# Kernel tuning notes

Measured on AMD Instinct MI355X. Metric: run time of the kernel, lower is better.

The kernel has to match this reference:

```python
import jax, jax.numpy as jnp
import numpy as np

B, L, D, T, NL = 64, 512, 512, 5000, 2


def setup_inputs() -> dict:
    key = jax.random.key(0)
    k1, k2, k3, k4 = jax.random.split(key, 4)
    enc_output = jax.random.normal(k1, (B, L, D), dtype=jnp.float32)
    # stands in for the row/col-normalized tag co-occurrence matrix (values in [0, 0.01])
    ui_adj = jax.random.uniform(k2, (T, T), dtype=jnp.float32) * 0.01
    # one GCN weight matrix per layer in the layer_stack
    Ws = jax.random.normal(k3, (NL, D, D), dtype=jnp.float32) / np.sqrt(D).astype(np.float32)
    # event ids are 1-indexed in the original (it indexes with e - 1)
    event_type = jax.random.randint(k4, (B, L), 1, T + 1, dtype=jnp.int64)
    slf_attn_mask = jnp.zeros((B, L, L), dtype=bool)
    non_pad_mask = jnp.ones((B, L), dtype=bool)
    return {"enc_output": enc_output, "ui_adj": ui_adj, "Ws": Ws,
            "event_type": event_type, "slf_attn_mask": slf_attn_mask,
            "non_pad_mask": non_pad_mask}


def reference(enc_output, ui_adj, Ws, event_type, slf_attn_mask, non_pad_mask):
    # --- batched per-sample adjacency gather (replaces the Python loop) ---
    idx = event_type - 1                                   # [B, L] 0-indexed
    sub = ui_adj[idx[:, :, None], idx[:, None, :]]         # [B, L, L] = ui_adj[e-1,:][:, e-1]
    diag = ui_adj[idx, idx]                                # [B, L]   = ui_adj[e-1, e-1]
    adj = sub + diag[:, None, :]                           # vector broadcasts across rows, as in torch
    # --- GNN layer stack (hGCN layer ~ relu(A @ X @ W)) ---
    x = enc_output
    for l in range(Ws.shape[0]):                           # small fixed n_layers loop
        x = jax.nn.relu(jnp.einsum('bij,bjd->bid', adj, x) @ Ws[l])
    # --- mean pool over sequence ---
    return x.mean(axis=1)                                  # [B, D]
```

## Files before the change

kernel.cpp:

```cpp
#include <hip/hip_runtime.h>

typedef unsigned short u16;
typedef unsigned int u32;
typedef __bf16 bf16x8 __attribute__((ext_vector_type(8)));
typedef float f32x4 __attribute__((ext_vector_type(4)));
typedef int i32x4 __attribute__((ext_vector_type(4)));
typedef u32 u32x2 __attribute__((ext_vector_type(2)));
typedef u32 u32x4 __attribute__((ext_vector_type(4)));

#define T_ 5000
#define CAP 96

__device__ __forceinline__ u16 f2bf(float f) {
  u32 u = __float_as_uint(f);
  u += 0x7fffu + ((u >> 16) & 1u);
  return (u16)(u >> 16);
}
__device__ __forceinline__ float bf2f(u32 bits16) {
  return __uint_as_float(bits16 << 16);
}

__device__ __forceinline__ void gload_lds16(const u16* g, u16* l) {
  __builtin_amdgcn_global_load_lds(
      (__attribute__((address_space(1))) void*)(u16*)g,
      (__attribute__((address_space(3))) void*)l, 16, 0, 0);
}

__device__ __forceinline__ u32 lds_off(const void* p) {
  return (u32)(uintptr_t)(__attribute__((address_space(3))) const void*)p;
}

__global__ void transpose_cast(const float* __restrict__ src, u16* __restrict__ dst) {
  __shared__ float tile[32][33];
  const int tx = threadIdx.x, ty = threadIdx.y;
  const int a0 = blockIdx.x * 32;
  const int b0 = blockIdx.y * 32;
  const size_t zoff = (size_t)blockIdx.z * (512 * 512);
  const float* s = src + zoff;
  u16* d = dst + zoff;
#pragma unroll
  for (int r = 0; r < 4; ++r)
    tile[ty + r * 8][tx] = s[(size_t)(a0 + ty + r * 8) * 512 + b0 + tx];
  __syncthreads();
#pragma unroll
  for (int r = 0; r < 4; ++r)
    d[(size_t)(b0 + ty + r * 8) * 512 + a0 + tx] = f2bf(tile[tx][ty + r * 8]);
}

__global__ void zero_k(int* __restrict__ cnt) {
  const int t = blockIdx.x * 256 + threadIdx.x;
  if (t < 5001) cnt[t] = 0;
}

__global__ void fill_k(const int* __restrict__ ev, const float* __restrict__ ui,
                       int2* __restrict__ cd, int* __restrict__ cnt,
                       int* __restrict__ list, int* __restrict__ ovf) {
  const int t = blockIdx.x * 256 + threadIdx.x;
  const int r = ev[t] - 1;
  int2 v;
  v.x = r;
  v.y = __float_as_int(ui[(size_t)r * (T_ + 1)]);
  cd[t] = v;
  const int pos = atomicAdd(&cnt[r], 1);
  if (pos < CAP) list[r * CAP + pos] = t;
  else { const int o = atomicAdd(&cnt[5000], 1); ovf[o] = t; }
}

__global__ __launch_bounds__(256)
void grow_gather(const float* __restrict__ ui, const int2* __restrict__ cd,
                 const int* __restrict__ cnt, const int* __restrict__ list,
                 u16* __restrict__ adj) {
  const int r = blockIdx.x;
  int c = cnt[r];
  if (c <= 0) return;
  if (c > CAP) c = CAP;
  __shared__ float row[5000];
  const float* __restrict__ src = ui + (size_t)r * T_;
  for (int t = threadIdx.x; t < 1250; t += 256)
    *(float4*)&row[t * 4] = *(const float4*)&src[t * 4];
  __syncthreads();
  const int j = threadIdx.x * 2;
  const int lb = r * CAP;
  int q = 0;
  for (; q + 2 <= c; q += 2) {
    const int t0 = list[lb + q], t1 = list[lb + q + 1];
    const int b0 = (t0 >> 9) << 9, b1 = (t1 >> 9) << 9;
    const int4 p0 = *(const int4*)&cd[b0 + j];
    const int4 p1 = *(const int4*)&cd[b1 + j];
    const u32 pk0 = (u32)f2bf(row[p0.x] + __int_as_float(p0.y)) |
                    ((u32)f2bf(row[p0.z] + __int_as_float(p0.w)) << 16);
    const u32 pk1 = (u32)f2bf(row[p1.x] + __int_as_float(p1.y)) |
                    ((u32)f2bf(row[p1.z] + __int_as_float(p1.w)) << 16);
    *(u32*)&adj[(size_t)t0 * 512 + j] = pk0;
    *(u32*)&adj[(size_t)t1 * 512 + j] = pk1;
  }
  if (q < c) {
    const int t0 = list[lb + q];
    const int b0 = (t0 >> 9) << 9;
    const int4 p0 = *(const int4*)&cd[b0 + j];
    const u32 pk0 = (u32)f2bf(row[p0.x] + __int_as_float(p0.y)) |
                    ((u32)f2bf(row[p0.z] + __int_as_float(p0.w)) << 16);
    *(u32*)&adj[(size_t)t0 * 512 + j] = pk0;
  }
}

__global__ void ovf_gather(const float* __restrict__ ui, const int2* __restrict__ cd,
                           const int* __restrict__ cnt, const int* __restrict__ ovf,
                           u16* __restrict__ adj) {
  const int n = cnt[5000];
  for (int q = blockIdx.x; q < n; q += gridDim.x) {
    const int t = ovf[q];
    const int base = (t >> 9) << 9;
    const long r = (long)cd[t].x;
    const float* __restrict__ row = ui + r * (long)T_;
    const int j = threadIdx.x * 2;
    const int4 p = *(const int4*)&cd[base + j];
    const u32 pk = (u32)f2bf(row[p.x] + __int_as_float(p.y)) |
                   ((u32)f2bf(row[p.z] + __int_as_float(p.w)) << 16);
    *(u32*)&adj[(size_t)t * 512 + j] = pk;
  }
}

template <int MODE, int BSRC>
__global__ __launch_bounds__(512, 2)
void gemm256(const u16* __restrict__ A, const void* __restrict__ Bv,
             u16* __restrict__ C, size_t strideA, size_t strideB, size_t strideC,
             float* __restrict__ P) {
  extern __shared__ u16 smem[];
  const int tid = threadIdx.x;
  const int lane = tid & 63;
  const int w = tid >> 6;
  const int wm = w >> 2, wn = w & 3;
  const int chunk = gridDim.x >> 3;
  const int wg = blockIdx.x;
  const int mapped = (wg & 7) * chunk + (wg >> 3);
  const int batch = mapped >> 2;
  const int tm = (mapped >> 1) & 1, tn = mapped & 1;
  const int m0 = tm << 8, n0 = tn << 8;
  const u16* __restrict__ Ab = A + (size_t)batch * strideA;

  const u16* gA[2];
  u32 ldA[2];
#pragma unroll
  for (int r = 0; r < 2; ++r) {
    const int c = r * 512 + tid;
    const int L = c * 16;
    const int pp = L >> 7;
    const int off = (L & 127) ^ ((pp & 7) << 4);
    const int m = pp * 2 + (off >> 6);
    const int kb = off & 63;
    gA[r] = Ab + (size_t)(m0 + m) * 512 + (kb >> 1);
    ldA[r] = (u32)((r * 512 + w * 64) * 8);
  }

  const u16* gB[2] = {nullptr, nullptr};
  u32 ldB[2] = {0, 0};
  if (BSRC == 0) {
    const u16* __restrict__ Bb = (const u16*)Bv + (size_t)batch * strideB;
#pragma unroll
    for (int r = 0; r < 2; ++r) {
      const int c = r * 512 + tid;
      const int L = c * 16;
      const int pp = L >> 7;
      const int off = (L & 127) ^ ((pp & 7) << 4);
      const int m = pp * 2 + (off >> 6);
      const int kb = off & 63;
      gB[r] = Bb + (size_t)(n0 + m) * 512 + (kb >> 1);
      ldB[r] = (u32)(32768 + (r * 512 + w * 64) * 8);
    }
  }

  const int dp = tid & 127;
  const int lq = tid >> 7;
  unsigned long long encB = 0;
  u32 boff0 = 0;
  u32x2 bs0[8], bs1[8];
  if (BSRC == 1) {
    encB = (unsigned long long)(uintptr_t)((const float*)Bv + (size_t)batch * strideB);
    boff0 = (u32)(((lq * 8) * 512 + n0 + dp * 2) * 4);
  }

#define BLOAD(t, S)                                                          \
  {                                                                          \
    const u32 ob = boff0 + (u32)(t) * 65536u;                                \
    _Pragma("unroll") for (int i = 0; i < 8; ++i)                            \
        asm volatile("global_load_dwordx2 %0, %1, %2"                        \
                     : "=v"(S[i])                                            \
                     : "v"(ob + (u32)i * 2048u), "s"(encB));                 \
  }

#define CONVERT_B(S)                                                         \
  {                                                                          \
    u32 wrd0[4], wrd1[4];                                                    \
    _Pragma("unroll") for (int jj = 0; jj < 4; ++jj) {                       \
      asm("v_cvt_pk_bf16_f32 %0, %1, %2"                                     \
          : "=v"(wrd0[jj]) : "v"(S[2 * jj].x), "v"(S[2 * jj + 1].x));        \
      asm("v_cvt_pk_bf16_f32 %0, %1, %2"                                     \
          : "=v"(wrd1[jj]) : "v"(S[2 * jj].y), "v"(S[2 * jj + 1].y));        \
    }                                                                        \
    const u32 by0 = (u32)dp * 128u + ((((u32)lq * 16u)) ^ (((u32)dp & 7u) << 4)); \
    const u32 by1 = (u32)dp * 128u + ((64u | ((u32)lq * 16u)) ^ (((u32)dp & 7u) << 4)); \
    u32x4 v0, v1;                                                            \
    v0.x = wrd0[0]; v0.y = wrd0[1]; v0.z = wrd0[2]; v0.w = wrd0[3];          \
    v1.x = wrd1[0]; v1.y = wrd1[1]; v1.z = wrd1[2]; v1.w = wrd1[3];          \
    *(u32x4*)((char*)smem + 65536 + by0) = v0;                               \
    *(u32x4*)((char*)smem + 65536 + by1) = v1;                               \
  }

  const int lr = lane & 15;
  const int kb = (lane >> 4) << 4;
  u32 aOff[8], bOff[4];
#pragma unroll
  for (int m = 0; m < 8; ++m) {
    const int row = wm * 128 + m * 16 + lr;
    aOff[m] = (u32)((row >> 1) * 128 + ((((row & 1) << 6) | kb) ^ (((row >> 1) & 7) << 4)));
  }
#pragma unroll
  for (int n = 0; n < 4; ++n) {
    const int row = wn * 64 + n * 16 + lr;
    bOff[n] = (u32)(65536 + (row >> 1) * 128 + ((((row & 1) << 6) | kb) ^ (((row >> 1) & 7) << 4)));
  }
  const u32 ldsBase = lds_off(smem);

  f32x4 acc[8][4] = {};

  auto stageA = [&](int t) {
    const u32 bo = (u32)(t & 3) * 8192;
#pragma unroll
    for (int r = 0; r < 2; ++r) gload_lds16(gA[r] + t * 32, smem + bo + ldA[r]);
  };
  auto stageB0 = [&](int t) {
    const u32 bo = (u32)(t & 3) * 8192;
#pragma unroll
    for (int r = 0; r < 2; ++r) gload_lds16(gB[r] + t * 32, smem + bo + ldB[r]);
  };

  if (BSRC == 0) {
    stageA(0); stageB0(0); stageA(1); stageB0(1); stageA(2); stageB0(2);
  } else {
    stageA(0); stageA(1); stageA(2);
    BLOAD(0, bs0); BLOAD(1, bs1);
  }

#pragma unroll
  for (int t = 0; t < 16; ++t) {
    if (BSRC == 0) {
      if (t <= 13)      asm volatile("s_waitcnt vmcnt(8)" ::: "memory");
      else if (t == 14) asm volatile("s_waitcnt vmcnt(4)" ::: "memory");
      else              asm volatile("s_waitcnt vmcnt(0)" ::: "memory");
      __builtin_amdgcn_sched_barrier(0);
      if (t + 3 < 16) { stageA(t + 3); stageB0(t + 3); }
      asm volatile("" ::: "memory");
      __builtin_amdgcn_s_barrier();
      asm volatile("" ::: "memory");
    } else {
      if (t == 0)              asm volatile("s_waitcnt vmcnt(8)" ::: "memory");
      else if (t <= 13)        asm volatile("s_waitcnt vmcnt(10)" ::: "memory");
      else if (t == 14)        asm volatile("s_waitcnt vmcnt(8)" ::: "memory");
      else                     asm volatile("s_waitcnt vmcnt(0)" ::: "memory");
      __builtin_amdgcn_sched_barrier(0);
      if (t & 1) { CONVERT_B(bs1); } else { CONVERT_B(bs0); }
      if (t + 3 < 16) stageA(t + 3);
      if (t + 2 < 16) { if (t & 1) { BLOAD(t + 2, bs1); } else { BLOAD(t + 2, bs0); } }
      asm volatile("s_waitcnt lgkmcnt(0)" ::: "memory");
      __builtin_amdgcn_s_barrier();
      asm volatile("" ::: "memory");
    }

    const u32 abase = ldsBase + (u32)(t & 3) * 16384;
    const u32 bbase = (BSRC == 0) ? (ldsBase + (u32)(t & 3) * 16384) : ldsBase;
    i32x4 araw[8], braw[4];
#pragma unroll
    for (int m = 0; m < 8; ++m)
      asm volatile("ds_read_b128 %0, %1" : "=v"(araw[m]) : "v"(abase + aOff[m]));
#pragma unroll
    for (int n = 0; n < 4; ++n)
      asm volatile("ds_read_b128 %0, %1" : "=v"(braw[n]) : "v"(bbase + bOff[n]));
    asm volatile("s_waitcnt lgkmcnt(0)" ::: "memory");
    __builtin_amdgcn_sched_barrier(0);

    __builtin_amdgcn_s_setprio(1);
#pragma unroll
    for (int m = 0; m < 8; ++m)
#pragma unroll
      for (int n = 0; n < 4; ++n)
        acc[m][n] = __builtin_amdgcn_mfma_f32_16x16x32_bf16(
            __builtin_bit_cast(bf16x8, araw[m]),
            __builtin_bit_cast(bf16x8, braw[n]), acc[m][n], 0, 0, 0);
    __builtin_amdgcn_s_setprio(0);
    asm volatile("" ::: "memory");
    __builtin_amdgcn_s_barrier();
    __builtin_amdgcn_sched_barrier(0);
  }
#undef BLOAD
#undef CONVERT_B

  u16* Cb = C + (size_t)batch * strideC;
  if (MODE == 0) {
#pragma unroll
    for (int m = 0; m < 8; ++m) {
      const int row = m0 + wm * 128 + m * 16 + (lane >> 4) * 4;
#pragma unroll
      for (int n = 0; n < 4; ++n) {
        const int col = n0 + wn * 64 + n * 16 + (lane & 15);
        const f32x4 v = acc[m][n];
#pragma unroll
        for (int j = 0; j < 4; ++j)
          Cb[(size_t)(row + j) * 512 + col] = f2bf(v[j]);
      }
    }
  } else if (MODE == 1) {
#pragma unroll
    for (int m = 0; m < 8; ++m) {
      const int i = m0 + wm * 128 + m * 16 + (lane >> 4) * 4;
#pragma unroll
      for (int n = 0; n < 4; ++n) {
        const int d = n0 + wn * 64 + n * 16 + (lane & 15);
        const f32x4 v = acc[m][n];
        uint2 p;
        p.x = (u32)f2bf(fmaxf(v[0], 0.f)) | ((u32)f2bf(fmaxf(v[1], 0.f)) << 16);
        p.y = (u32)f2bf(fmaxf(v[2], 0.f)) | ((u32)f2bf(fmaxf(v[3], 0.f)) << 16);
        *(uint2*)&Cb[(size_t)d * 512 + i] = p;
      }
    }
  } else {
    const int slot = tm * 2 + wm;
#pragma unroll
    for (int n = 0; n < 4; ++n) {
      float s = 0.f;
#pragma unroll
      for (int m = 0; m < 8; ++m) {
        const f32x4 v = acc[m][n];
#pragma unroll
        for (int j = 0; j < 4; ++j) s += fmaxf(v[j], 0.f);
      }
      s += __shfl_xor(s, 16);
      s += __shfl_xor(s, 32);
      if ((lane >> 4) == 0) {
        const int d = n0 + wn * 64 + n * 16 + lane;
        P[((size_t)batch * 4 + slot) * 512 + d] = s;
      }
    }
  }
}

__global__ void reduce_mean(const float* __restrict__ P, float* __restrict__ out) {
  const int t = blockIdx.x * 256 + threadIdx.x;
  const int b = t >> 9, d = t & 511;
  float s = 0.f;
#pragma unroll
  for (int q = 0; q < 4; ++q) s += P[((size_t)b * 4 + q) * 512 + d];
  out[t] = s * (1.0f / 512.0f);
}

extern "C" void kernel_launch(void* const* d_in, const int* in_sizes, int n_in,
                              void* d_out, int out_size, void* d_ws, size_t ws_size,
                              hipStream_t stream) {
  const float* enc = (const float*)d_in[0];
  const float* ui  = (const float*)d_in[1];
  const float* Ws  = (const float*)d_in[2];
  const int*   ev  = (const int*)d_in[3];
  float* out = (float*)d_out;

  char* ws = (char*)d_ws;
  const size_t SLAB = (size_t)64 * 512 * 512 * 2;
  u16* adj  = (u16*)(ws);
  u16* tbuf = (u16*)(ws + SLAB);
  u16* xb   = (u16*)(ws + 2 * SLAB);
  char* p = ws + 3 * SLAB;
  u16* wst  = (u16*)p;  p += (size_t)2 * 512 * 512 * 2;
  int2* cd  = (int2*)p; p += (size_t)32768 * 8;
  int* cnt  = (int*)p;  p += 5008 * 4;
  int* list = (int*)p;  p += (size_t)5000 * CAP * 4;
  int* ovf  = (int*)p;  p += (size_t)32768 * 4;
  float* P  = (float*)p;

  const size_t PS = (size_t)512 * 512;
  const size_t SMEM0 = 131072;
  const size_t SMEM1 = 81920;
  (void)hipFuncSetAttribute(reinterpret_cast<const void*>(gemm256<0, 1>),
                            hipFuncAttributeMaxDynamicSharedMemorySize, (int)SMEM1);
  (void)hipFuncSetAttribute(reinterpret_cast<const void*>(gemm256<1, 0>),
                            hipFuncAttributeMaxDynamicSharedMemorySize, (int)SMEM0);
  (void)hipFuncSetAttribute(reinterpret_cast<const void*>(gemm256<0, 0>),
                            hipFuncAttributeMaxDynamicSharedMemorySize, (int)SMEM0);
  (void)hipFuncSetAttribute(reinterpret_cast<const void*>(gemm256<2, 0>),
                            hipFuncAttributeMaxDynamicSharedMemorySize, (int)SMEM0);

  zero_k<<<20, 256, 0, stream>>>(cnt);
  fill_k<<<128, 256, 0, stream>>>(ev, ui, cd, cnt, list, ovf);
  transpose_cast<<<dim3(16, 16, 2), dim3(32, 8), 0, stream>>>(Ws, wst);
  grow_gather<<<5000, 256, 0, stream>>>(ui, cd, cnt, list, adj);
  ovf_gather<<<8, 256, 0, stream>>>(ui, cd, cnt, ovf, adj);
  gemm256<0, 1><<<256, 512, SMEM1, stream>>>(adj, enc, tbuf, PS, PS, PS, nullptr);
  gemm256<1, 0><<<256, 512, SMEM0, stream>>>(tbuf, wst, xb, PS, 0, PS, nullptr);
  gemm256<0, 0><<<256, 512, SMEM0, stream>>>(adj, xb, tbuf, PS, PS, PS, nullptr);
  gemm256<2, 0><<<256, 512, SMEM0, stream>>>(tbuf, wst + PS, nullptr, PS, 0, 0, P);
  reduce_mean<<<128, 256, 0, stream>>>(P, out);
}
```

Baseline: 141.1 us.

## Switch GEMMs to 32x32x16 MFMA, split LDS waits, and merge small launches

The GEMM inner loop moves from 16x16x32 to 32x32x16 bf16 MFMA tiles, so fewer LDS fragment reads feed the same work. The LDS wait is split so the first half of the MFMAs can start after a partial lgkmcnt wait. The three epilogues are remapped to the 32x32 accumulator layout. Separately, counter zeroing is folded into the weight transpose kernel, and the overflow gather is folded into grow_gather, which also stages its list in LDS and unrolls by four. This removes two kernel launches but makes blocks 0-7 do the overflow work serially.

```diff
diff --git a/kernel.cpp b/kernel.cpp
--- a/kernel.cpp
+++ b/kernel.cpp
@@ -3,7 +3,7 @@
 typedef unsigned short u16;
 typedef unsigned int u32;
 typedef __bf16 bf16x8 __attribute__((ext_vector_type(8)));
-typedef float f32x4 __attribute__((ext_vector_type(4)));
+typedef float f32x16 __attribute__((ext_vector_type(16)));
 typedef int i32x4 __attribute__((ext_vector_type(4)));
 typedef u32 u32x2 __attribute__((ext_vector_type(2)));
 typedef u32 u32x4 __attribute__((ext_vector_type(4)));
@@ -30,7 +30,13 @@
   return (u32)(uintptr_t)(__attribute__((address_space(3))) const void*)p;
 }
 
-__global__ void transpose_cast(const float* __restrict__ src, u16* __restrict__ dst) {
+__device__ __forceinline__ u32 swz(int row, int kb) {
+  return (u32)((row >> 1) * 128 +
+               ((((row & 1) << 6) | kb) ^ (((row >> 1) & 7) << 4)));
+}
+
+__global__ void prep_k(const float* __restrict__ src, u16* __restrict__ dst,
+                       int* __restrict__ cnt) {
   __shared__ float tile[32][33];
   const int tx = threadIdx.x, ty = threadIdx.y;
   const int a0 = blockIdx.x * 32;
@@ -41,15 +47,12 @@
 #pragma unroll
   for (int r = 0; r < 4; ++r)
     tile[ty + r * 8][tx] = s[(size_t)(a0 + ty + r * 8) * 512 + b0 + tx];
+  const int gid = ((blockIdx.z * 16 + blockIdx.y) * 16 + blockIdx.x) * 256 + ty * 32 + tx;
+  if (gid < 5008) cnt[gid] = 0;
   __syncthreads();
 #pragma unroll
   for (int r = 0; r < 4; ++r)
     d[(size_t)(b0 + ty + r * 8) * 512 + a0 + tx] = f2bf(tile[tx][ty + r * 8]);
-}
-
-__global__ void zero_k(int* __restrict__ cnt) {
-  const int t = blockIdx.x * 256 + threadIdx.x;
-  if (t < 5001) cnt[t] = 0;
 }
 
 __global__ void fill_k(const int* __restrict__ ev, const float* __restrict__ ui,
@@ -69,55 +72,58 @@
 __global__ __launch_bounds__(256)
 void grow_gather(const float* __restrict__ ui, const int2* __restrict__ cd,
                  const int* __restrict__ cnt, const int* __restrict__ list,
-                 u16* __restrict__ adj) {
+                 const int* __restrict__ ovf, u16* __restrict__ adj) {
+  __shared__ float row[5000];
+  __shared__ int lst[CAP];
   const int r = blockIdx.x;
   int c = cnt[r];
-  if (c <= 0) return;
   if (c > CAP) c = CAP;
-  __shared__ float row[5000];
-  const float* __restrict__ src = ui + (size_t)r * T_;
-  for (int t = threadIdx.x; t < 1250; t += 256)
-    *(float4*)&row[t * 4] = *(const float4*)&src[t * 4];
-  __syncthreads();
   const int j = threadIdx.x * 2;
-  const int lb = r * CAP;
-  int q = 0;
-  for (; q + 2 <= c; q += 2) {
-    const int t0 = list[lb + q], t1 = list[lb + q + 1];
-    const int b0 = (t0 >> 9) << 9, b1 = (t1 >> 9) << 9;
-    const int4 p0 = *(const int4*)&cd[b0 + j];
-    const int4 p1 = *(const int4*)&cd[b1 + j];
-    const u32 pk0 = (u32)f2bf(row[p0.x] + __int_as_float(p0.y)) |
-                    ((u32)f2bf(row[p0.z] + __int_as_float(p0.w)) << 16);
-    const u32 pk1 = (u32)f2bf(row[p1.x] + __int_as_float(p1.y)) |
-                    ((u32)f2bf(row[p1.z] + __int_as_float(p1.w)) << 16);
-    *(u32*)&adj[(size_t)t0 * 512 + j] = pk0;
-    *(u32*)&adj[(size_t)t1 * 512 + j] = pk1;
-  }
-  if (q < c) {
-    const int t0 = list[lb + q];
-    const int b0 = (t0 >> 9) << 9;
-    const int4 p0 = *(const int4*)&cd[b0 + j];
-    const u32 pk0 = (u32)f2bf(row[p0.x] + __int_as_float(p0.y)) |
-                    ((u32)f2bf(row[p0.z] + __int_as_float(p0.w)) << 16);
-    *(u32*)&adj[(size_t)t0 * 512 + j] = pk0;
-  }
-}
-
-__global__ void ovf_gather(const float* __restrict__ ui, const int2* __restrict__ cd,
-                           const int* __restrict__ cnt, const int* __restrict__ ovf,
-                           u16* __restrict__ adj) {
-  const int n = cnt[5000];
-  for (int q = blockIdx.x; q < n; q += gridDim.x) {
-    const int t = ovf[q];
-    const int base = (t >> 9) << 9;
-    const long r = (long)cd[t].x;
-    const float* __restrict__ row = ui + r * (long)T_;
-    const int j = threadIdx.x * 2;
-    const int4 p = *(const int4*)&cd[base + j];
-    const u32 pk = (u32)f2bf(row[p.x] + __int_as_float(p.y)) |
-                   ((u32)f2bf(row[p.z] + __int_as_float(p.w)) << 16);
-    *(u32*)&adj[(size_t)t * 512 + j] = pk;
+  if (c > 0) {
+    const float* __restrict__ src = ui + (size_t)r * T_;
+    for (int t = threadIdx.x; t < 1250; t += 256)
+      *(float4*)&row[t * 4] = *(const float4*)&src[t * 4];
+    if (threadIdx.x < c) lst[threadIdx.x] = list[r * CAP + threadIdx.x];
+    __syncthreads();
+    int q = 0;
+    for (; q + 4 <= c; q += 4) {
+      const int t0 = lst[q], t1 = lst[q + 1], t2 = lst[q + 2], t3 = lst[q + 3];
+      const int4 p0 = *(const int4*)&cd[((t0 >> 9) << 9) + j];
+      const int4 p1 = *(const int4*)&cd[((t1 >> 9) << 9) + j];
+      const int4 p2 = *(const int4*)&cd[((t2 >> 9) << 9) + j];
+      const int4 p3 = *(const int4*)&cd[((t3 >> 9) << 9) + j];
+      const u32 k0 = (u32)f2bf(row[p0.x] + __int_as_float(p0.y)) |
+                     ((u32)f2bf(row[p0.z] + __int_as_float(p0.w)) << 16);
+      const u32 k1 = (u32)f2bf(row[p1.x] + __int_as_float(p1.y)) |
+                     ((u32)f2bf(row[p1.z] + __int_as_float(p1.w)) << 16);
+      const u32 k2 = (u32)f2bf(row[p2.x] + __int_as_float(p2.y)) |
+                     ((u32)f2bf(row[p2.z] + __int_as_float(p2.w)) << 16);
+      const u32 k3 = (u32)f2bf(row[p3.x] + __int_as_float(p3.y)) |
+                     ((u32)f2bf(row[p3.z] + __int_as_float(p3.w)) << 16);
+      *(u32*)&adj[(size_t)t0 * 512 + j] = k0;
+      *(u32*)&adj[(size_t)t1 * 512 + j] = k1;
+      *(u32*)&adj[(size_t)t2 * 512 + j] = k2;
+      *(u32*)&adj[(size_t)t3 * 512 + j] = k3;
+    }
+    for (; q < c; ++q) {
+      const int t0 = lst[q];
+      const int4 p0 = *(const int4*)&cd[((t0 >> 9) << 9) + j];
+      const u32 k0 = (u32)f2bf(row[p0.x] + __int_as_float(p0.y)) |
+                     ((u32)f2bf(row[p0.z] + __int_as_float(p0.w)) << 16);
+      *(u32*)&adj[(size_t)t0 * 512 + j] = k0;
+    }
+  }
+  if (r < 8) {
+    const int n = cnt[5000];
+    for (int q = r; q < n; q += 8) {
+      const int t = ovf[q];
+      const long rr = (long)cd[t].x;
+      const float* __restrict__ rp = ui + rr * (long)T_;
+      const int4 p = *(const int4*)&cd[((t >> 9) << 9) + j];
+      const u32 pk = (u32)f2bf(rp[p.x] + __int_as_float(p.y)) |
+                     ((u32)f2bf(rp[p.z] + __int_as_float(p.w)) << 16);
+      *(u32*)&adj[(size_t)t * 512 + j] = pk;
+    }
   }
 }
 
@@ -207,22 +213,22 @@
     *(u32x4*)((char*)smem + 65536 + by1) = v1;                               \
   }
 
-  const int lr = lane & 15;
-  const int kb = (lane >> 4) << 4;
-  u32 aOff[8], bOff[4];
-#pragma unroll
-  for (int m = 0; m < 8; ++m) {
-    const int row = wm * 128 + m * 16 + lr;
-    aOff[m] = (u32)((row >> 1) * 128 + ((((row & 1) << 6) | kb) ^ (((row >> 1) & 7) << 4)));
-  }
-#pragma unroll
-  for (int n = 0; n < 4; ++n) {
-    const int row = wn * 64 + n * 16 + lr;
-    bOff[n] = (u32)(65536 + (row >> 1) * 128 + ((((row & 1) << 6) | kb) ^ (((row >> 1) & 7) << 4)));
-  }
+  const int col = lane & 31;
+  const int h16 = (lane >> 5) * 16;
+  u32 aOff[4][2], bOff[2][2];
+#pragma unroll
+  for (int mf = 0; mf < 4; ++mf)
+#pragma unroll
+    for (int kk = 0; kk < 2; ++kk)
+      aOff[mf][kk] = swz(wm * 128 + mf * 32 + col, kk * 32 + h16);
+#pragma unroll
+  for (int nf = 0; nf < 2; ++nf)
+#pragma unroll
+    for (int kk = 0; kk < 2; ++kk)
+      bOff[nf][kk] = 65536u + swz(wn * 64 + nf * 32 + col, kk * 32 + h16);
   const u32 ldsBase = lds_off(smem);
 
-  f32x4 acc[8][4] = {};
+  f32x16 acc[4][2] = {};
 
   auto stageA = [&](int t) {
     const u32 bo = (u32)(t & 3) * 8192;
@@ -268,25 +274,47 @@
     }
 
     const u32 abase = ldsBase + (u32)(t & 3) * 16384;
-    const u32 bbase = (BSRC == 0) ? (ldsBase + (u32)(t & 3) * 16384) : ldsBase;
-    i32x4 araw[8], braw[4];
-#pragma unroll
-    for (int m = 0; m < 8; ++m)
-      asm volatile("ds_read_b128 %0, %1" : "=v"(araw[m]) : "v"(abase + aOff[m]));
-#pragma unroll
-    for (int n = 0; n < 4; ++n)
-      asm volatile("ds_read_b128 %0, %1" : "=v"(braw[n]) : "v"(bbase + bOff[n]));
+    const u32 bbase = (BSRC == 0) ? abase : ldsBase;
+    i32x4 braw[2][2], araw[4][2];
+#pragma unroll
+    for (int nf = 0; nf < 2; ++nf)
+#pragma unroll
+      for (int kk = 0; kk < 2; ++kk)
+        asm volatile("ds_read_b128 %0, %1" : "=v"(braw[nf][kk]) : "v"(bbase + bOff[nf][kk]));
+#pragma unroll
+    for (int mf = 0; mf < 2; ++mf)
+#pragma unroll
+      for (int kk = 0; kk < 2; ++kk)
+        asm volatile("ds_read_b128 %0, %1" : "=v"(araw[mf][kk]) : "v"(abase + aOff[mf][kk]));
+#pragma unroll
+    for (int mf = 2; mf < 4; ++mf)
+#pragma unroll
+      for (int kk = 0; kk < 2; ++kk)
+        asm volatile("ds_read_b128 %0, %1" : "=v"(araw[mf][kk]) : "v"(abase + aOff[mf][kk]));
+
+    asm volatile("s_waitcnt lgkmcnt(4)" ::: "memory");
+    __builtin_amdgcn_sched_barrier(0);
+    __builtin_amdgcn_s_setprio(1);
+#pragma unroll
+    for (int kk = 0; kk < 2; ++kk)
+#pragma unroll
+      for (int mf = 0; mf < 2; ++mf)
+#pragma unroll
+        for (int nf = 0; nf < 2; ++nf)
+          acc[mf][nf] = __builtin_amdgcn_mfma_f32_32x32x16_bf16(
+              __builtin_bit_cast(bf16x8, araw[mf][kk]),
+              __builtin_bit_cast(bf16x8, braw[nf][kk]), acc[mf][nf], 0, 0, 0);
     asm volatile("s_waitcnt lgkmcnt(0)" ::: "memory");
     __builtin_amdgcn_sched_barrier(0);
-
-    __builtin_amdgcn_s_setprio(1);
-#pragma unroll
-    for (int m = 0; m < 8; ++m)
-#pragma unroll
-      for (int n = 0; n < 4; ++n)
-        acc[m][n] = __builtin_amdgcn_mfma_f32_16x16x32_bf16(
-            __builtin_bit_cast(bf16x8, araw[m]),
-            __builtin_bit_cast(bf16x8, braw[n]), acc[m][n], 0, 0, 0);
+#pragma unroll
+    for (int kk = 0; kk < 2; ++kk)
+#pragma unroll
+      for (int mf = 2; mf < 4; ++mf)
+#pragma unroll
+        for (int nf = 0; nf < 2; ++nf)
+          acc[mf][nf] = __builtin_amdgcn_mfma_f32_32x32x16_bf16(
+              __builtin_bit_cast(bf16x8, araw[mf][kk]),
+              __builtin_bit_cast(bf16x8, braw[nf][kk]), acc[mf][nf], 0, 0, 0);
     __builtin_amdgcn_s_setprio(0);
     asm volatile("" ::: "memory");
     __builtin_amdgcn_s_barrier();
@@ -298,46 +326,53 @@
   u16* Cb = C + (size_t)batch * strideC;
   if (MODE == 0) {
 #pragma unroll
-    for (int m = 0; m < 8; ++m) {
-      const int row = m0 + wm * 128 + m * 16 + (lane >> 4) * 4;
-#pragma unroll
-      for (int n = 0; n < 4; ++n) {
-        const int col = n0 + wn * 64 + n * 16 + (lane & 15);
-        const f32x4 v = acc[m][n];
-#pragma unroll
-        for (int j = 0; j < 4; ++j)
-          Cb[(size_t)(row + j) * 512 + col] = f2bf(v[j]);
+    for (int mf = 0; mf < 4; ++mf) {
+      const int rbase = m0 + wm * 128 + mf * 32 + 4 * (lane >> 5);
+#pragma unroll
+      for (int nf = 0; nf < 2; ++nf) {
+        const int cc = n0 + wn * 64 + nf * 32 + col;
+        const f32x16 v = acc[mf][nf];
+#pragma unroll
+        for (int g = 0; g < 4; ++g)
+#pragma unroll
+          for (int j = 0; j < 4; ++j)
+            Cb[(size_t)(rbase + 8 * g + j) * 512 + cc] = f2bf(v[g * 4 + j]);
       }
     }
   } else if (MODE == 1) {
 #pragma unroll
-    for (int m = 0; m < 8; ++m) {
-      const int i = m0 + wm * 128 + m * 16 + (lane >> 4) * 4;
-#pragma unroll
-      for (int n = 0; n < 4; ++n) {
-        const int d = n0 + wn * 64 + n * 16 + (lane & 15);
-        const f32x4 v = acc[m][n];
-        uint2 p;
-        p.x = (u32)f2bf(fmaxf(v[0], 0.f)) | ((u32)f2bf(fmaxf(v[1], 0.f)) << 16);
-        p.y = (u32)f2bf(fmaxf(v[2], 0.f)) | ((u32)f2bf(fmaxf(v[3], 0.f)) << 16);
-        *(uint2*)&Cb[(size_t)d * 512 + i] = p;
+    for (int mf = 0; mf < 4; ++mf) {
+      const int ibase = m0 + wm * 128 + mf * 32 + 4 * (lane >> 5);
+#pragma unroll
+      for (int nf = 0; nf < 2; ++nf) {
+        const int d = n0 + wn * 64 + nf * 32 + col;
+        const f32x16 v = acc[mf][nf];
+#pragma unroll
+        for (int g = 0; g < 4; ++g) {
+          const int i = ibase + 8 * g;
+          uint2 p;
+          p.x = (u32)f2bf(fmaxf(v[g * 4 + 0], 0.f)) |
+                ((u32)f2bf(fmaxf(v[g * 4 + 1], 0.f)) << 16);
+          p.y = (u32)f2bf(fmaxf(v[g * 4 + 2], 0.f)) |
+                ((u32)f2bf(fmaxf(v[g * 4 + 3], 0.f)) << 16);
+          *(uint2*)&Cb[(size_t)d * 512 + i] = p;
+        }
       }
     }
   } else {
     const int slot = tm * 2 + wm;
 #pragma unroll
-    for (int n = 0; n < 4; ++n) {
+    for (int nf = 0; nf < 2; ++nf) {
       float s = 0.f;
 #pragma unroll
-      for (int m = 0; m < 8; ++m) {
-        const f32x4 v = acc[m][n];
-#pragma unroll
-        for (int j = 0; j < 4; ++j) s += fmaxf(v[j], 0.f);
+      for (int mf = 0; mf < 4; ++mf) {
+        const f32x16 v = acc[mf][nf];
+#pragma unroll
+        for (int r = 0; r < 16; ++r) s += fmaxf(v[r], 0.f);
       }
-      s += __shfl_xor(s, 16);
       s += __shfl_xor(s, 32);
-      if ((lane >> 4) == 0) {
-        const int d = n0 + wn * 64 + n * 16 + lane;
+      if (lane < 32) {
+        const int d = n0 + wn * 64 + nf * 32 + lane;
         P[((size_t)batch * 4 + slot) * 512 + d] = s;
       }
     }
@@ -387,11 +422,9 @@
   (void)hipFuncSetAttribute(reinterpret_cast<const void*>(gemm256<2, 0>),
                             hipFuncAttributeMaxDynamicSharedMemorySize, (int)SMEM0);
 
-  zero_k<<<20, 256, 0, stream>>>(cnt);
+  prep_k<<<dim3(16, 16, 2), dim3(32, 8), 0, stream>>>(Ws, wst, cnt);
   fill_k<<<128, 256, 0, stream>>>(ev, ui, cd, cnt, list, ovf);
-  transpose_cast<<<dim3(16, 16, 2), dim3(32, 8), 0, stream>>>(Ws, wst);
-  grow_gather<<<5000, 256, 0, stream>>>(ui, cd, cnt, list, adj);
-  ovf_gather<<<8, 256, 0, stream>>>(ui, cd, cnt, ovf, adj);
+  grow_gather<<<5000, 256, 0, stream>>>(ui, cd, cnt, list, ovf, adj);
   gemm256<0, 1><<<256, 512, SMEM1, stream>>>(adj, enc, tbuf, PS, PS, PS, nullptr);
   gemm256<1, 0><<<256, 512, SMEM0, stream>>>(tbuf, wst, xb, PS, 0, PS, nullptr);
   gemm256<0, 0><<<256, 512, SMEM0, stream>>>(adj, xb, tbuf, PS, PS, PS, nullptr);
```

Result: slower. 144.9 us (+2.7%).
